# Optimization experiments

Hardware: AMD Instinct MI355X
Metric: run time of the kernel (lower is better)

## Reference

```python
import jax, jax.numpy as jnp
import numpy as np

S, B, D = 2048, 32, 1024
H = 16
DIM = D // H  # 64 per-head dim
EPS = 1e-5


def setup_inputs() -> dict:
    key = jax.random.key(0)
    k1, k2, k3 = jax.random.split(key, 3)
    src = jax.random.normal(k1, (S, B, D), dtype=jnp.float32)
    # per-head bracket Linear(2*dim -> dim), stacked over heads
    bound = 1.0 / np.sqrt(2 * DIM)
    W = jax.random.uniform(k2, (H, 2 * DIM, DIM), minval=-bound, maxval=bound, dtype=jnp.float32)
    b = jax.random.uniform(k3, (H, DIM), minval=-bound, maxval=bound, dtype=jnp.float32)
    # shared LayerNorm(d_model) params (default init: gamma=1, beta=0)
    gamma = jnp.ones((D,), dtype=jnp.float32)
    beta = jnp.zeros((D,), dtype=jnp.float32)
    return {"src": src, "W": W, "b": b, "gamma": gamma, "beta": beta}


def reference(src, W, b, gamma, beta):
    def layer_norm(x):
        mu = jnp.mean(x, axis=-1, keepdims=True)
        var = jnp.mean(jnp.square(x - mu), axis=-1, keepdims=True)
        return (x - mu) * jax.lax.rsqrt(var + EPS) * gamma + beta

    def step(c, x):
        # c, x: [B, D]; mode='base': y_h = GELU(Linear_h([c_h; x_h])), new context = x
        ch = c.reshape(B, H, DIM)
        xh = x.reshape(B, H, DIM)
        cat = jnp.concatenate([ch, xh], axis=-1)              # [B, H, 2*DIM]
        y = jax.nn.gelu(jnp.einsum('bhk,hkd->bhd', cat, W) + b, approximate=False)
        c_new = layer_norm(x)                                  # LN(context)=LN(x)
        y_out = layer_norm(y.reshape(B, D))
        return c_new, y_out

    c0 = jnp.zeros((B, D), dtype=src.dtype)
    _, ys = jax.lax.scan(step, c0, src)
    return ys  # [S, B, D]
```

## Files before the change

kernel.cpp:

```cpp
#include <hip/hip_runtime.h>

#define SS 2048
#define BB 32
#define DD 1024
#define RB 8

typedef unsigned short u16;
typedef unsigned int u32;
using f32x4 = __attribute__((ext_vector_type(4))) float;
using bf16x8 = __attribute__((ext_vector_type(8))) short;

__device__ __forceinline__ u16 f2bf(float x) {
  union { float f; u32 u; } c; c.f = x;
  u32 r = c.u + 0x7fffu + ((c.u >> 16) & 1u);
  return (u16)(r >> 16);
}
__device__ __forceinline__ int swzb(int row, int col) {
  return ((row << 11) + (col << 1)) ^ ((row & 7) << 4);
}
__device__ __forceinline__ void st8(u16* base, int row, int col, float4 a, float4 b) {
  uint4 pk;
  pk.x = (u32)f2bf(a.x) | ((u32)f2bf(a.y) << 16);
  pk.y = (u32)f2bf(a.z) | ((u32)f2bf(a.w) << 16);
  pk.z = (u32)f2bf(b.x) | ((u32)f2bf(b.y) << 16);
  pk.w = (u32)f2bf(b.z) | ((u32)f2bf(b.w) << 16);
  *reinterpret_cast<uint4*>(reinterpret_cast<char*>(base) + swzb(row, col)) = pk;
}
__device__ __forceinline__ void st8z(u16* base, int row, int col) {
  uint4 pk; pk.x = pk.y = pk.z = pk.w = 0u;
  *reinterpret_cast<uint4*>(reinterpret_cast<char*>(base) + swzb(row, col)) = pk;
}
__device__ __forceinline__ bf16x8 ld_afrag(const u16* base, int row, int col) {
  return *reinterpret_cast<const bf16x8*>(reinterpret_cast<const char*>(base) + swzb(row, col));
}
__device__ __forceinline__ float gelu_f(float v) {
  const float u2 = 1.5957691216057308f * v * __builtin_fmaf(0.044715f, v * v, 1.0f);
  const float e = __expf(u2);
  const float th = 1.0f - 2.0f * __builtin_amdgcn_rcpf(e + 1.0f);
  return 0.5f * v * (1.0f + th);
}
__device__ __forceinline__ void rowstats(float4 a, float4 b, float4 c, float4 d,
                                         float& mu, float& rs) {
  float s1 = a.x + a.y + a.z + a.w + b.x + b.y + b.z + b.w +
             c.x + c.y + c.z + c.w + d.x + d.y + d.z + d.w;
  float s2 = a.x*a.x + a.y*a.y + a.z*a.z + a.w*a.w + b.x*b.x + b.y*b.y + b.z*b.z + b.w*b.w +
             c.x*c.x + c.y*c.y + c.z*c.z + c.w*c.w + d.x*d.x + d.y*d.y + d.z*d.z + d.w*d.w;
#pragma unroll
  for (int off = 32; off; off >>= 1) { s1 += __shfl_xor(s1, off); s2 += __shfl_xor(s2, off); }
  mu = s1 * (1.f / 1024.f);
  rs = rsqrtf(s2 * (1.f / 1024.f) - mu * mu + 1e-5f);
}

__global__ void prep_w2(const float* __restrict__ W, const float* __restrict__ gamma,
                        u16* __restrict__ Wf) {
  const int o = blockIdx.x * 256 + threadIdx.x;
  const int l = o & 63;
  const int tile = o >> 6;
  const int nt = tile & 3, ks = (tile >> 2) & 3, h = tile >> 4;
  const int d = nt * 16 + (l & 15);
  const int kbw = ks * 32 + 8 * (l >> 4);
  u16 v[8];
#pragma unroll
  for (int j = 0; j < 8; ++j) {
    const int k = kbw + j;
    float w = W[(h * 128 + k) * 64 + d];
    if (ks < 2) w *= gamma[h * 64 + k];
    v[j] = f2bf(w);
  }
  uint4 pk;
  pk.x = (u32)v[0] | ((u32)v[1] << 16);
  pk.y = (u32)v[2] | ((u32)v[3] << 16);
  pk.z = (u32)v[4] | ((u32)v[5] << 16);
  pk.w = (u32)v[6] | ((u32)v[7] << 16);
  reinterpret_cast<uint4*>(Wf)[o] = pk;
}

__global__ void prep_v(const float* __restrict__ W, const float* __restrict__ gamma,
                       const float* __restrict__ beta, const float* __restrict__ bias,
                       float* __restrict__ vg, float* __restrict__ bias2) {
  const int d = blockIdx.x * 256 + threadIdx.x;
  const int h = d >> 6, dd = d & 63;
  float sg = 0.f, sb = 0.f;
  for (int k = 0; k < 64; ++k) {
    const float w = W[(h * 128 + k) * 64 + dd];
    sg += gamma[h * 64 + k] * w;
    sb += beta[h * 64 + k] * w;
  }
  vg[d] = sg;
  bias2[d] = bias[d] + sb;
}

__global__ __launch_bounds__(256, 4) void lienet_main(
    const float* __restrict__ src, const u16* __restrict__ Wf,
    const float* __restrict__ vg, const float* __restrict__ bias2,
    const float* __restrict__ bias, const float* __restrict__ gamma,
    const float* __restrict__ beta, float* __restrict__ out) {
  __shared__ __align__(16) u16 cbuf[RB * DD];
  __shared__ __align__(16) u16 xbuf[RB * DD];
  __shared__ float part[4][RB][2];
  __shared__ float pm[RB];

  const int bid = blockIdx.x;
  const int lin = (bid & 7) * 1024 + (bid >> 3);
  const int t = lin >> 2;
  const int rg = lin & 3;

  const int tid = threadIdx.x;
  const int wave = tid >> 6;
  const int lane = tid & 63;
  const int c0 = lane * 16;
  const uint4* wfu = reinterpret_cast<const uint4*>(Wf);

#pragma unroll
  for (int rr = 0; rr < 2; ++rr) {
    const int row = wave * 2 + rr;
    const int grow = rg * RB + row;
    const float* xp = src + ((size_t)t * BB + grow) * DD + c0;
    float4 x0 = *reinterpret_cast<const float4*>(xp);
    float4 x1 = *reinterpret_cast<const float4*>(xp + 4);
    float4 x2 = *reinterpret_cast<const float4*>(xp + 8);
    float4 x3 = *reinterpret_cast<const float4*>(xp + 12);
    if (t > 0) {
      const float* cp = src + ((size_t)(t - 1) * BB + grow) * DD + c0;
      float4 y0 = *reinterpret_cast<const float4*>(cp);
      float4 y1 = *reinterpret_cast<const float4*>(cp + 4);
      float4 y2 = *reinterpret_cast<const float4*>(cp + 8);
      float4 y3 = *reinterpret_cast<const float4*>(cp + 12);
      st8(xbuf, row, c0, x0, x1);
      st8(xbuf, row, c0 + 8, x2, x3);
      float pmu, ps;
      rowstats(y0, y1, y2, y3, pmu, ps);
      y0.x *= ps; y0.y *= ps; y0.z *= ps; y0.w *= ps;
      y1.x *= ps; y1.y *= ps; y1.z *= ps; y1.w *= ps;
      y2.x *= ps; y2.y *= ps; y2.z *= ps; y2.w *= ps;
      y3.x *= ps; y3.y *= ps; y3.z *= ps; y3.w *= ps;
      st8(cbuf, row, c0, y0, y1);
      st8(cbuf, row, c0 + 8, y2, y3);
      if (lane == 0) pm[row] = pmu * ps;
    } else {
      st8(xbuf, row, c0, x0, x1);
      st8(xbuf, row, c0 + 8, x2, x3);
      st8z(cbuf, row, c0);
      st8z(cbuf, row, c0 + 8);
      if (lane == 0) pm[row] = 0.f;
    }
  }
  __syncthreads();

  f32x4 acc[4][4];
#pragma unroll
  for (int hh = 0; hh < 4; ++hh)
#pragma unroll
    for (int nt = 0; nt < 4; ++nt) acc[hh][nt] = (f32x4){0.f, 0.f, 0.f, 0.f};

  const int arow = lane & 7;
  const int kb = 8 * (lane >> 4);
#pragma unroll
  for (int ks = 0; ks < 4; ++ks) {
    const u16* sb = (ks < 2) ? cbuf : xbuf;
#pragma unroll
    for (int hh = 0; hh < 4; ++hh) {
      const int h = wave * 4 + hh;
      bf16x8 a = ld_afrag(sb, arow, h * 64 + (ks & 1) * 32 + kb);
      const uint4* wp = wfu + ((h * 4 + ks) * 4) * 64 + lane;
#pragma unroll
      for (int nt = 0; nt < 4; ++nt) {
        uint4 wv = wp[nt * 64];
        acc[hh][nt] = __builtin_amdgcn_mfma_f32_16x16x32_bf16(
            a, *reinterpret_cast<bf16x8*>(&wv), acc[hh][nt], 0, 0, 0);
      }
    }
  }

  const int hilo = lane >> 5;
  const int row4 = 4 * ((lane >> 4) & 1);
  const int cl = lane & 15;
  const float* bptr = (t == 0) ? bias : bias2;
  float pmv[4];
#pragma unroll
  for (int r = 0; r < 4; ++r) pmv[r] = pm[row4 + r];
  float gv[2][4][4];
#pragma unroll
  for (int hp = 0; hp < 2; ++hp) {
    const int h_eff = wave * 4 + hp + 2 * hilo;
#pragma unroll
    for (int nt = 0; nt < 4; ++nt) {
      const int d = h_eff * 64 + nt * 16 + cl;
      const float bt = bptr[d];
      const float vgv = vg[d];
#pragma unroll
      for (int r = 0; r < 4; ++r) {
        const float v = (hilo ? acc[hp + 2][nt][r] : acc[hp][nt][r]) + bt - pmv[r] * vgv;
        gv[hp][nt][r] = gelu_f(v);
      }
    }
  }
  float s1[4], s2[4];
#pragma unroll
  for (int r = 0; r < 4; ++r) {
    float a = 0.f, b = 0.f;
#pragma unroll
    for (int hp = 0; hp < 2; ++hp)
#pragma unroll
      for (int nt = 0; nt < 4; ++nt) {
        const float g = gv[hp][nt][r];
        a += g; b += g * g;
      }
    a += __shfl_xor(a, 1); b += __shfl_xor(b, 1);
    a += __shfl_xor(a, 2); b += __shfl_xor(b, 2);
    a += __shfl_xor(a, 4); b += __shfl_xor(b, 4);
    a += __shfl_xor(a, 8); b += __shfl_xor(b, 8);
    a += __shfl_xor(a, 32); b += __shfl_xor(b, 32);
    s1[r] = a; s2[r] = b;
  }
  if (lane == 0 || lane == 16) {
#pragma unroll
    for (int r = 0; r < 4; ++r) {
      part[wave][row4 + r][0] = s1[r];
      part[wave][row4 + r][1] = s2[r];
    }
  }
  float gm[2][4], bt2[2][4];
#pragma unroll
  for (int hp = 0; hp < 2; ++hp) {
    const int h_eff = wave * 4 + hp + 2 * hilo;
#pragma unroll
    for (int nt = 0; nt < 4; ++nt) {
      const int d = h_eff * 64 + nt * 16 + cl;
      gm[hp][nt] = gamma[d];
      bt2[hp][nt] = beta[d];
    }
  }
  __syncthreads();

#pragma unroll
  for (int r = 0; r < 4; ++r) {
    const int row = row4 + r;
    const float a = part[0][row][0] + part[1][row][0] + part[2][row][0] + part[3][row][0];
    const float b = part[0][row][1] + part[1][row][1] + part[2][row][1] + part[3][row][1];
    const float mu = a * (1.f / 1024.f);
    const float rs = rsqrtf(b * (1.f / 1024.f) - mu * mu + 1e-5f);
    float* op = out + ((size_t)t * BB + rg * RB + row) * DD;
#pragma unroll
    for (int hp = 0; hp < 2; ++hp) {
      const int h_eff = wave * 4 + hp + 2 * hilo;
#pragma unroll
      for (int nt = 0; nt < 4; ++nt)
        op[h_eff * 64 + nt * 16 + cl] = (gv[hp][nt][r] - mu) * rs * gm[hp][nt] + bt2[hp][nt];
    }
  }
}

extern "C" void kernel_launch(void* const* d_in, const int* in_sizes, int n_in,
                              void* d_out, int out_size, void* d_ws, size_t ws_size,
                              hipStream_t stream) {
  const float* src = (const float*)d_in[0];
  const float* W = (const float*)d_in[1];
  const float* bias = (const float*)d_in[2];
  const float* gamma = (const float*)d_in[3];
  const float* beta = (const float*)d_in[4];
  float* out = (float*)d_out;
  u16* Wf = (u16*)d_ws;
  float* vgp = (float*)((char*)d_ws + 262144);
  float* b2p = vgp + 1024;

  prep_w2<<<64, 256, 0, stream>>>(W, gamma, Wf);
  prep_v<<<4, 256, 0, stream>>>(W, gamma, beta, bias, vgp, b2p);
  lienet_main<<<SS * 4, 256, 0, stream>>>(src, Wf, vgp, b2p, bias, gamma, beta, out);
}
```

Before: 222.7 us.

## Process two consecutive timesteps per block, reusing x row as next context

Each block now handles two adjacent timesteps instead of one, halving the grid. The x rows loaded for the first step are reused, via their bf16 shared-memory copy and precomputed LayerNorm scale, as the context for the second step. This removes one global read of the previous row per pair and halves per-block setup overhead. In exchange the second step's context is rebuilt from bf16-rounded x rather than fp32, which may change rounding slightly. It also adds an extra barrier and serialises the two steps inside one block.

Result: slower. 884.7 us (+297.2%).

```diff
diff --git a/kernel.cpp b/kernel.cpp
--- a/kernel.cpp
+++ b/kernel.cpp
@@ -14,6 +14,9 @@
   union { float f; u32 u; } c; c.f = x;
   u32 r = c.u + 0x7fffu + ((c.u >> 16) & 1u);
   return (u16)(r >> 16);
+}
+__device__ __forceinline__ float bf2f(u32 h) {
+  union { u32 u; float f; } c; c.u = h << 16; return c.f;
 }
 __device__ __forceinline__ int swzb(int row, int col) {
   return ((row << 11) + (col << 1)) ^ ((row & 7) << 4);
@@ -29,6 +32,9 @@
 __device__ __forceinline__ void st8z(u16* base, int row, int col) {
   uint4 pk; pk.x = pk.y = pk.z = pk.w = 0u;
   *reinterpret_cast<uint4*>(reinterpret_cast<char*>(base) + swzb(row, col)) = pk;
+}
+__device__ __forceinline__ uint4 ld16(const u16* base, int row, int col) {
+  return *reinterpret_cast<const uint4*>(reinterpret_cast<const char*>(base) + swzb(row, col));
 }
 __device__ __forceinline__ bf16x8 ld_afrag(const u16* base, int row, int col) {
   return *reinterpret_cast<const bf16x8*>(reinterpret_cast<const char*>(base) + swzb(row, col));
@@ -101,8 +107,8 @@
   __shared__ float pm[RB];
 
   const int bid = blockIdx.x;
-  const int lin = (bid & 7) * 1024 + (bid >> 3);
-  const int t = lin >> 2;
+  const int lin = (bid & 7) * 512 + (bid >> 3);
+  const int t0 = (lin >> 2) * 2;
   const int rg = lin & 3;
 
   const int tid = threadIdx.x;
@@ -111,23 +117,34 @@
   const int c0 = lane * 16;
   const uint4* wfu = reinterpret_cast<const uint4*>(Wf);
 
+  const int hilo = lane >> 5;
+  const int row4 = 4 * ((lane >> 4) & 1);
+  const int cl = lane & 15;
+  const int arow = lane & 7;
+  const int kb = 8 * (lane >> 4);
+
+  float cur_s[2], cur_pm[2];
+
 #pragma unroll
   for (int rr = 0; rr < 2; ++rr) {
     const int row = wave * 2 + rr;
     const int grow = rg * RB + row;
-    const float* xp = src + ((size_t)t * BB + grow) * DD + c0;
+    const float* xp = src + ((size_t)t0 * BB + grow) * DD + c0;
     float4 x0 = *reinterpret_cast<const float4*>(xp);
     float4 x1 = *reinterpret_cast<const float4*>(xp + 4);
     float4 x2 = *reinterpret_cast<const float4*>(xp + 8);
     float4 x3 = *reinterpret_cast<const float4*>(xp + 12);
-    if (t > 0) {
-      const float* cp = src + ((size_t)(t - 1) * BB + grow) * DD + c0;
+    float xmu, xrs;
+    if (t0 > 0) {
+      const float* cp = src + ((size_t)(t0 - 1) * BB + grow) * DD + c0;
       float4 y0 = *reinterpret_cast<const float4*>(cp);
       float4 y1 = *reinterpret_cast<const float4*>(cp + 4);
       float4 y2 = *reinterpret_cast<const float4*>(cp + 8);
       float4 y3 = *reinterpret_cast<const float4*>(cp + 12);
       st8(xbuf, row, c0, x0, x1);
       st8(xbuf, row, c0 + 8, x2, x3);
+      rowstats(x0, x1, x2, x3, xmu, xrs);
+      cur_s[rr] = xrs; cur_pm[rr] = xmu * xrs;
       float pmu, ps;
       rowstats(y0, y1, y2, y3, pmu, ps);
       y0.x *= ps; y0.y *= ps; y0.z *= ps; y0.w *= ps;
@@ -140,6 +157,8 @@
     } else {
       st8(xbuf, row, c0, x0, x1);
       st8(xbuf, row, c0 + 8, x2, x3);
+      rowstats(x0, x1, x2, x3, xmu, xrs);
+      cur_s[rr] = xrs; cur_pm[rr] = xmu * xrs;
       st8z(cbuf, row, c0);
       st8z(cbuf, row, c0 + 8);
       if (lane == 0) pm[row] = 0.f;
@@ -147,106 +166,136 @@
   }
   __syncthreads();
 
-  f32x4 acc[4][4];
-#pragma unroll
-  for (int hh = 0; hh < 4; ++hh)
-#pragma unroll
-    for (int nt = 0; nt < 4; ++nt) acc[hh][nt] = (f32x4){0.f, 0.f, 0.f, 0.f};
-
-  const int arow = lane & 7;
-  const int kb = 8 * (lane >> 4);
-#pragma unroll
-  for (int ks = 0; ks < 4; ++ks) {
-    const u16* sb = (ks < 2) ? cbuf : xbuf;
-#pragma unroll
-    for (int hh = 0; hh < 4; ++hh) {
-      const int h = wave * 4 + hh;
-      bf16x8 a = ld_afrag(sb, arow, h * 64 + (ks & 1) * 32 + kb);
-      const uint4* wp = wfu + ((h * 4 + ks) * 4) * 64 + lane;
-#pragma unroll
-      for (int nt = 0; nt < 4; ++nt) {
-        uint4 wv = wp[nt * 64];
-        acc[hh][nt] = __builtin_amdgcn_mfma_f32_16x16x32_bf16(
-            a, *reinterpret_cast<bf16x8*>(&wv), acc[hh][nt], 0, 0, 0);
-      }
-    }
-  }
-
-  const int hilo = lane >> 5;
-  const int row4 = 4 * ((lane >> 4) & 1);
-  const int cl = lane & 15;
-  const float* bptr = (t == 0) ? bias : bias2;
-  float pmv[4];
-#pragma unroll
-  for (int r = 0; r < 4; ++r) pmv[r] = pm[row4 + r];
-  float gv[2][4][4];
-#pragma unroll
-  for (int hp = 0; hp < 2; ++hp) {
-    const int h_eff = wave * 4 + hp + 2 * hilo;
-#pragma unroll
-    for (int nt = 0; nt < 4; ++nt) {
-      const int d = h_eff * 64 + nt * 16 + cl;
-      const float bt = bptr[d];
-      const float vgv = vg[d];
-#pragma unroll
-      for (int r = 0; r < 4; ++r) {
-        const float v = (hilo ? acc[hp + 2][nt][r] : acc[hp][nt][r]) + bt - pmv[r] * vgv;
-        gv[hp][nt][r] = gelu_f(v);
-      }
-    }
-  }
-  float s1[4], s2[4];
-#pragma unroll
-  for (int r = 0; r < 4; ++r) {
-    float a = 0.f, b = 0.f;
-#pragma unroll
-    for (int hp = 0; hp < 2; ++hp)
-#pragma unroll
-      for (int nt = 0; nt < 4; ++nt) {
-        const float g = gv[hp][nt][r];
-        a += g; b += g * g;
-      }
-    a += __shfl_xor(a, 1); b += __shfl_xor(b, 1);
-    a += __shfl_xor(a, 2); b += __shfl_xor(b, 2);
-    a += __shfl_xor(a, 4); b += __shfl_xor(b, 4);
-    a += __shfl_xor(a, 8); b += __shfl_xor(b, 8);
-    a += __shfl_xor(a, 32); b += __shfl_xor(b, 32);
-    s1[r] = a; s2[r] = b;
-  }
-  if (lane == 0 || lane == 16) {
-#pragma unroll
-    for (int r = 0; r < 4; ++r) {
-      part[wave][row4 + r][0] = s1[r];
-      part[wave][row4 + r][1] = s2[r];
-    }
-  }
-  float gm[2][4], bt2[2][4];
-#pragma unroll
-  for (int hp = 0; hp < 2; ++hp) {
-    const int h_eff = wave * 4 + hp + 2 * hilo;
-#pragma unroll
-    for (int nt = 0; nt < 4; ++nt) {
-      const int d = h_eff * 64 + nt * 16 + cl;
-      gm[hp][nt] = gamma[d];
-      bt2[hp][nt] = beta[d];
-    }
-  }
-  __syncthreads();
-
-#pragma unroll
-  for (int r = 0; r < 4; ++r) {
-    const int row = row4 + r;
-    const float a = part[0][row][0] + part[1][row][0] + part[2][row][0] + part[3][row][0];
-    const float b = part[0][row][1] + part[1][row][1] + part[2][row][1] + part[3][row][1];
-    const float mu = a * (1.f / 1024.f);
-    const float rs = rsqrtf(b * (1.f / 1024.f) - mu * mu + 1e-5f);
-    float* op = out + ((size_t)t * BB + rg * RB + row) * DD;
+  for (int ph = 0; ph < 2; ++ph) {
+    const int t = t0 + ph;
+
+    f32x4 acc[4][4];
+#pragma unroll
+    for (int hh = 0; hh < 4; ++hh)
+#pragma unroll
+      for (int nt = 0; nt < 4; ++nt) acc[hh][nt] = (f32x4){0.f, 0.f, 0.f, 0.f};
+
+#pragma unroll
+    for (int ks = 0; ks < 4; ++ks) {
+      const u16* sb = (ks < 2) ? cbuf : xbuf;
+#pragma unroll
+      for (int hh = 0; hh < 4; ++hh) {
+        const int h = wave * 4 + hh;
+        bf16x8 a = ld_afrag(sb, arow, h * 64 + (ks & 1) * 32 + kb);
+        const uint4* wp = wfu + ((h * 4 + ks) * 4) * 64 + lane;
+#pragma unroll
+        for (int nt = 0; nt < 4; ++nt) {
+          uint4 wv = wp[nt * 64];
+          acc[hh][nt] = __builtin_amdgcn_mfma_f32_16x16x32_bf16(
+              a, *reinterpret_cast<bf16x8*>(&wv), acc[hh][nt], 0, 0, 0);
+        }
+      }
+    }
+
+    const float* bptr = (t == 0) ? bias : bias2;
+    float pmv[4];
+#pragma unroll
+    for (int r = 0; r < 4; ++r) pmv[r] = pm[row4 + r];
+    float gv[2][4][4];
 #pragma unroll
     for (int hp = 0; hp < 2; ++hp) {
       const int h_eff = wave * 4 + hp + 2 * hilo;
 #pragma unroll
-      for (int nt = 0; nt < 4; ++nt)
-        op[h_eff * 64 + nt * 16 + cl] = (gv[hp][nt][r] - mu) * rs * gm[hp][nt] + bt2[hp][nt];
+      for (int nt = 0; nt < 4; ++nt) {
+        const int d = h_eff * 64 + nt * 16 + cl;
+        const float bt = bptr[d];
+        const float vgv = vg[d];
+#pragma unroll
+        for (int r = 0; r < 4; ++r) {
+          const float v = (hilo ? acc[hp + 2][nt][r] : acc[hp][nt][r]) + bt - pmv[r] * vgv;
+          gv[hp][nt][r] = gelu_f(v);
+        }
+      }
+    }
+    float s1[4], s2[4];
+#pragma unroll
+    for (int r = 0; r < 4; ++r) {
+      float a = 0.f, b = 0.f;
+#pragma unroll
+      for (int hp = 0; hp < 2; ++hp)
+#pragma unroll
+        for (int nt = 0; nt < 4; ++nt) {
+          const float g = gv[hp][nt][r];
+          a += g; b += g * g;
+        }
+      a += __shfl_xor(a, 1); b += __shfl_xor(b, 1);
+      a += __shfl_xor(a, 2); b += __shfl_xor(b, 2);
+      a += __shfl_xor(a, 4); b += __shfl_xor(b, 4);
+      a += __shfl_xor(a, 8); b += __shfl_xor(b, 8);
+      a += __shfl_xor(a, 32); b += __shfl_xor(b, 32);
+      s1[r] = a; s2[r] = b;
+    }
+    if (lane == 0 || lane == 16) {
+#pragma unroll
+      for (int r = 0; r < 4; ++r) {
+        part[wave][row4 + r][0] = s1[r];
+        part[wave][row4 + r][1] = s2[r];
+      }
+    }
+    float gm[2][4], bt2[2][4];
+#pragma unroll
+    for (int hp = 0; hp < 2; ++hp) {
+      const int h_eff = wave * 4 + hp + 2 * hilo;
+#pragma unroll
+      for (int nt = 0; nt < 4; ++nt) {
+        const int d = h_eff * 64 + nt * 16 + cl;
+        gm[hp][nt] = gamma[d];
+        bt2[hp][nt] = beta[d];
+      }
+    }
+    __syncthreads();
+
+#pragma unroll
+    for (int r = 0; r < 4; ++r) {
+      const int row = row4 + r;
+      const float a = part[0][row][0] + part[1][row][0] + part[2][row][0] + part[3][row][0];
+      const float b = part[0][row][1] + part[1][row][1] + part[2][row][1] + part[3][row][1];
+      const float mu = a * (1.f / 1024.f);
+      const float rs = rsqrtf(b * (1.f / 1024.f) - mu * mu + 1e-5f);
+      float* op = out + ((size_t)t * BB + rg * RB + row) * DD;
+#pragma unroll
+      for (int hp = 0; hp < 2; ++hp) {
+        const int h_eff = wave * 4 + hp + 2 * hilo;
+#pragma unroll
+        for (int nt = 0; nt < 4; ++nt)
+          op[h_eff * 64 + nt * 16 + cl] = (gv[hp][nt][r] - mu) * rs * gm[hp][nt] + bt2[hp][nt];
+      }
+    }
+
+    if (ph == 0) {
+#pragma unroll
+      for (int rr = 0; rr < 2; ++rr) {
+        const int row = wave * 2 + rr;
+        const int grow = rg * RB + row;
+        const float* xp = src + ((size_t)(t0 + 1) * BB + grow) * DD + c0;
+        float4 n0 = *reinterpret_cast<const float4*>(xp);
+        float4 n1 = *reinterpret_cast<const float4*>(xp + 4);
+        float4 n2 = *reinterpret_cast<const float4*>(xp + 8);
+        float4 n3 = *reinterpret_cast<const float4*>(xp + 12);
+        const float sc = cur_s[rr];
+        uint4 g0 = ld16(xbuf, row, c0);
+        uint4 g1 = ld16(xbuf, row, c0 + 8);
+        float4 a0, a1, a2, a3;
+        a0.x = bf2f(g0.x & 0xffffu) * sc; a0.y = bf2f(g0.x >> 16) * sc;
+        a0.z = bf2f(g0.y & 0xffffu) * sc; a0.w = bf2f(g0.y >> 16) * sc;
+        a1.x = bf2f(g0.z & 0xffffu) * sc; a1.y = bf2f(g0.z >> 16) * sc;
+        a1.z = bf2f(g0.w & 0xffffu) * sc; a1.w = bf2f(g0.w >> 16) * sc;
+        a2.x = bf2f(g1.x & 0xffffu) * sc; a2.y = bf2f(g1.x >> 16) * sc;
+        a2.z = bf2f(g1.y & 0xffffu) * sc; a2.w = bf2f(g1.y >> 16) * sc;
+        a3.x = bf2f(g1.z & 0xffffu) * sc; a3.y = bf2f(g1.z >> 16) * sc;
+        a3.z = bf2f(g1.w & 0xffffu) * sc; a3.w = bf2f(g1.w >> 16) * sc;
+        st8(cbuf, row, c0, a0, a1);
+        st8(cbuf, row, c0 + 8, a2, a3);
+        if (lane == 0) pm[row] = cur_pm[rr];
+        st8(xbuf, row, c0, n0, n1);
+        st8(xbuf, row, c0 + 8, n2, n3);
+      }
+      __syncthreads();
     }
   }
 }
@@ -266,5 +315,5 @@
 
   prep_w2<<<64, 256, 0, stream>>>(W, gamma, Wf);
   prep_v<<<4, 256, 0, stream>>>(W, gamma, beta, bias, vgp, b2p);
-  lienet_main<<<SS * 4, 256, 0, stream>>>(src, Wf, vgp, b2p, bias, gamma, beta, out);
-}
+  lienet_main<<<SS * 2, 256, 0, stream>>>(src, Wf, vgp, b2p, bias, gamma, beta, out);
+}
```
